# Kernel optimization log

Measured on AMD Instinct MI355X. Metric: run time of the kernel, lower is better.

The kernel has to match this reference:

```python
import jax, jax.numpy as jnp
import numpy as np

D_IN, D_HID, D_CLS, N_CLASSES = 1024, 256, 128, 4
CELL_IN = 512
N = 50000


def setup_inputs() -> dict:
    key = jax.random.key(0)
    ks = jax.random.split(key, 20)
    s = 0.02
    inp = {
        "x_path": jax.random.normal(ks[0], (1, N, D_IN), jnp.float32),
        "x_cell": jax.random.normal(ks[1], (1, N, CELL_IN), jnp.float32),
        # wsi_net / cell_net projections
        "wsi_w": jax.random.normal(ks[2], (D_IN, D_HID), jnp.float32) * s,
        "wsi_b": jnp.zeros((D_HID,), jnp.float32),
        "cell_w": jax.random.normal(ks[3], (CELL_IN, D_HID), jnp.float32) * s,
        "cell_b": jnp.zeros((D_HID,), jnp.float32),
        # cross-attention Q/K/V
        "wq_w": jax.random.normal(ks[4], (D_HID, D_HID), jnp.float32) * s,
        "wq_b": jnp.zeros((D_HID,), jnp.float32),
        "wk_w": jax.random.normal(ks[5], (D_HID, D_HID), jnp.float32) * s,
        "wk_b": jnp.zeros((D_HID,), jnp.float32),
        "wv_w": jax.random.normal(ks[6], (D_HID, D_HID), jnp.float32) * s,
        "wv_b": jnp.zeros((D_HID,), jnp.float32),
        # gated attention (L=D=256, n_classes=1)
        "aa_w": jax.random.normal(ks[7], (D_HID, D_HID), jnp.float32) * s,
        "aa_b": jnp.zeros((D_HID,), jnp.float32),
        "ab_w": jax.random.normal(ks[8], (D_HID, D_HID), jnp.float32) * s,
        "ab_b": jnp.zeros((D_HID,), jnp.float32),
        "ac_w": jax.random.normal(ks[9], (D_HID, 1), jnp.float32) * s,
        "ac_b": jnp.zeros((1,), jnp.float32),
        # classifier MLP
        "c1_w": jax.random.normal(ks[10], (D_HID, D_CLS), jnp.float32) * s,
        "c1_b": jnp.zeros((D_CLS,), jnp.float32),
        "c2_w": jax.random.normal(ks[11], (D_CLS, N_CLASSES), jnp.float32) * s,
        "c2_b": jnp.zeros((N_CLASSES,), jnp.float32),
    }
    return inp


def reference(x_path, x_cell, wsi_w, wsi_b, cell_w, cell_b,
              wq_w, wq_b, wk_w, wk_b, wv_w, wv_b,
              aa_w, aa_b, ab_w, ab_b, ac_w, ac_b,
              c1_w, c1_b, c2_w, c2_b):
    xp = x_path[0]            # (N, D_IN)
    xc = x_cell[0]            # (N, CELL_IN)
    # instance-level projections (dropout inactive at eval)
    h_path = jax.nn.relu(xp @ wsi_w + wsi_b)    # (N, d)
    h_cell = jax.nn.relu(xc @ cell_w + cell_b)  # (N, d)
    # cross attention with per-instance seq_len=1 (bmm over N singleton batches)
    q = h_cell @ wq_w + wq_b
    k = h_path @ wk_w + wk_b
    v = h_path @ wv_w + wv_b
    scores = (jnp.einsum('nd,nd->n', q, k) / jnp.sqrt(jnp.float32(q.shape[-1])))[:, None, None]  # (N,1,1)
    attn_w = jax.nn.softmax(scores, axis=-1)     # (N,1,1), trivially ones
    fused = attn_w[:, 0, :] * v                  # (N, d)
    # gated attention MIL pooling
    a = jnp.tanh(fused @ aa_w + aa_b)
    b = jax.nn.sigmoid(fused @ ab_w + ab_b)
    A = (a * b) @ ac_w + ac_b                    # (N, 1)
    A_t = A.T                                    # (1, N)
    pooled = jax.nn.softmax(A_t, axis=1) @ fused # (1, d)
    # classifier MLP
    risk = jax.nn.relu(pooled @ c1_w + c1_b) @ c2_w + c2_b  # (1, n_classes)
    return risk
```

## Files before the change

kernel.cpp:

```cpp
#include <hip/hip_runtime.h>
#include <hip/hip_bf16.h>
#include <math.h>

#define D_IN 1024
#define D_HID 256
#define D_CLS 128
#define N_CLASSES 4
#define N_INST 50000

#define ROWS 64
#define NBLK ((N_INST + ROWS - 1) / ROWS)
#define NB2 64
#define CHUNK ((NBLK + NB2 - 1) / NB2)
#define NEG_BIG (-1e30f)

typedef __attribute__((ext_vector_type(8))) short bf16x8;
typedef __attribute__((ext_vector_type(4))) float f32x4;

__global__ void convert_weights(const float* __restrict__ w1, const float* __restrict__ wv,
                                const float* __restrict__ wa, const float* __restrict__ wb,
                                __hip_bfloat16* __restrict__ w1t, __hip_bfloat16* __restrict__ wvt,
                                __hip_bfloat16* __restrict__ wat, __hip_bfloat16* __restrict__ wbt) {
    int idx = blockIdx.x * 256 + threadIdx.x;
    if (idx < D_IN * D_HID) {
        int k = idx >> 8;
        int n = idx & 255;
        w1t[(size_t)n * D_IN + k] = __float2bfloat16(w1[idx]);
    }
    if (idx < D_HID * D_HID) {
        int k = idx >> 8, n = idx & 255;
        wvt[n * D_HID + k] = __float2bfloat16(wv[idx]);
        wat[n * D_HID + k] = __float2bfloat16(wa[idx]);
        wbt[n * D_HID + k] = __float2bfloat16(wb[idx]);
    }
}

__device__ __forceinline__ void gemm256(const __hip_bfloat16 (*S)[264],
                                        const __hip_bfloat16* __restrict__ Wt,
                                        int wave, int quad, int l16, f32x4 acc[4][4]) {
    f32x4 zero = {0.f, 0.f, 0.f, 0.f};
#pragma unroll
    for (int i = 0; i < 4; i++)
#pragma unroll
        for (int j = 0; j < 4; j++) acc[i][j] = zero;
#pragma unroll
    for (int ks = 0; ks < 8; ks++) {
        bf16x8 af[4];
#pragma unroll
        for (int rt = 0; rt < 4; rt++)
            af[rt] = *(const bf16x8*)&S[rt * 16 + l16][ks * 32 + quad * 8];
#pragma unroll
        for (int ct = 0; ct < 4; ct++) {
            bf16x8 bf = *(const bf16x8*)(Wt + (size_t)(wave * 64 + ct * 16 + l16) * D_HID + ks * 32 + quad * 8);
#pragma unroll
            for (int rt = 0; rt < 4; rt++)
                acc[rt][ct] = __builtin_amdgcn_mfma_f32_16x16x32_bf16(af[rt], bf, acc[rt][ct], 0, 0, 0);
        }
    }
}

__launch_bounds__(256, 2)
__global__ void mcat_main(const float* __restrict__ xp,
                          const __hip_bfloat16* __restrict__ w1t, const float* __restrict__ b1,
                          const __hip_bfloat16* __restrict__ wvt, const float* __restrict__ bv,
                          const __hip_bfloat16* __restrict__ wat, const float* __restrict__ ba,
                          const __hip_bfloat16* __restrict__ wbt, const float* __restrict__ bb,
                          const float* __restrict__ acw, const float* __restrict__ acb,
                          float* __restrict__ partials) {
    __shared__ __hip_bfloat16 Xs[ROWS][72];
    __shared__ __hip_bfloat16 Hs[ROWS][264];
    __shared__ __hip_bfloat16 Vs[ROWS][264];
    __shared__ float Apart[4][ROWS];
    __shared__ float ExpW[ROWS];

    const int tid  = threadIdx.x;
    const int wave = tid >> 6;
    const int lane = tid & 63;
    const int quad = lane >> 4;
    const int l16  = lane & 15;
    const int row0 = blockIdx.x * ROWS;

    f32x4 acc[4][4];
    f32x4 zero = {0.f, 0.f, 0.f, 0.f};
#pragma unroll
    for (int i = 0; i < 4; i++)
#pragma unroll
        for (int j = 0; j < 4; j++) acc[i][j] = zero;

    for (int kc = 0; kc < D_IN; kc += 64) {
#pragma unroll
        for (int i = 0; i < 4; i++) {
            int lin = (i << 8) + tid;
            int r = lin >> 4;
            int c4 = (lin & 15) << 2;
            int grow = row0 + r;
            float4 xv = {0.f, 0.f, 0.f, 0.f};
            if (grow < N_INST) xv = *(const float4*)(xp + (size_t)grow * D_IN + kc + c4);
            Xs[r][c4 + 0] = __float2bfloat16(xv.x);
            Xs[r][c4 + 1] = __float2bfloat16(xv.y);
            Xs[r][c4 + 2] = __float2bfloat16(xv.z);
            Xs[r][c4 + 3] = __float2bfloat16(xv.w);
        }
        __syncthreads();
#pragma unroll
        for (int ks = 0; ks < 2; ks++) {
            bf16x8 af[4];
#pragma unroll
            for (int rt = 0; rt < 4; rt++)
                af[rt] = *(const bf16x8*)&Xs[rt * 16 + l16][ks * 32 + quad * 8];
#pragma unroll
            for (int ct = 0; ct < 4; ct++) {
                bf16x8 bf = *(const bf16x8*)(w1t + (size_t)(wave * 64 + ct * 16 + l16) * D_IN + kc + ks * 32 + quad * 8);
#pragma unroll
                for (int rt = 0; rt < 4; rt++)
                    acc[rt][ct] = __builtin_amdgcn_mfma_f32_16x16x32_bf16(af[rt], bf, acc[rt][ct], 0, 0, 0);
            }
        }
        __syncthreads();
    }
#pragma unroll
    for (int ct = 0; ct < 4; ct++) {
        int col = wave * 64 + ct * 16 + l16;
        float bias = b1[col];
#pragma unroll
        for (int rt = 0; rt < 4; rt++)
#pragma unroll
            for (int r = 0; r < 4; r++) {
                int row = rt * 16 + quad * 4 + r;
                float h = acc[rt][ct][r] + bias;
                Hs[row][col] = __float2bfloat16(fmaxf(h, 0.f));
            }
    }
    __syncthreads();

    gemm256(Hs, wvt, wave, quad, l16, acc);
#pragma unroll
    for (int ct = 0; ct < 4; ct++) {
        int col = wave * 64 + ct * 16 + l16;
        float bias = bv[col];
#pragma unroll
        for (int rt = 0; rt < 4; rt++)
#pragma unroll
            for (int r = 0; r < 4; r++) {
                int row = rt * 16 + quad * 4 + r;
                Vs[row][col] = __float2bfloat16(acc[rt][ct][r] + bias);
            }
    }
    __syncthreads();

    gemm256(Vs, wat, wave, quad, l16, acc);
#pragma unroll
    for (int ct = 0; ct < 4; ct++) {
        int col = wave * 64 + ct * 16 + l16;
        float bias = ba[col];
#pragma unroll
        for (int rt = 0; rt < 4; rt++)
#pragma unroll
            for (int r = 0; r < 4; r++) {
                int row = rt * 16 + quad * 4 + r;
                Hs[row][col] = __float2bfloat16(tanhf(acc[rt][ct][r] + bias));
            }
    }

    gemm256(Vs, wbt, wave, quad, l16, acc);
#pragma unroll
    for (int ct = 0; ct < 4; ct++) {
        int col = wave * 64 + ct * 16 + l16;
        float bias = bb[col];
#pragma unroll
        for (int rt = 0; rt < 4; rt++)
#pragma unroll
            for (int r = 0; r < 4; r++) {
                int row = rt * 16 + quad * 4 + r;
                float bval = 1.f / (1.f + __expf(-(acc[rt][ct][r] + bias)));
                float aval = __bfloat162float(Hs[row][col]);
                Hs[row][col] = __float2bfloat16(aval * bval);
            }
    }
    __syncthreads();

    {
        int r = tid & 63;
        int dg = tid >> 6;
        float s = 0.f;
#pragma unroll 8
        for (int d = 0; d < 64; d++) {
            int col = dg * 64 + d;
            s += __bfloat162float(Hs[r][col]) * acw[col];
        }
        Apart[dg][r] = s;
    }
    __syncthreads();

    if (tid < 64) {
        bool valid = (row0 + tid) < N_INST;
        float A = Apart[0][tid] + Apart[1][tid] + Apart[2][tid] + Apart[3][tid] + acb[0];
        if (!valid) A = NEG_BIG;
        float m = A;
#pragma unroll
        for (int off = 32; off > 0; off >>= 1) m = fmaxf(m, __shfl_xor(m, off));
        float e = valid ? __expf(A - m) : 0.f;
        ExpW[tid] = e;
        float ssum = e;
#pragma unroll
        for (int off = 32; off > 0; off >>= 1) ssum += __shfl_xor(ssum, off);
        if (tid == 0) {
            partials[(size_t)blockIdx.x * 258 + 0] = m;
            partials[(size_t)blockIdx.x * 258 + 1] = ssum;
        }
    }
    __syncthreads();
    {
        float p = 0.f;
#pragma unroll 8
        for (int n = 0; n < 64; n++)
            p += ExpW[n] * __bfloat162float(Vs[n][tid]);
        partials[(size_t)blockIdx.x * 258 + 2 + tid] = p;
    }
}

__global__ void mcat_fin_a(const float* __restrict__ p1, float* __restrict__ p2) {
    __shared__ float sm[1];
    int g = blockIdx.x, tid = threadIdx.x;
    int lo = g * CHUNK;
    int hi = lo + CHUNK; if (hi > NBLK) hi = NBLK;
    if (tid < 64) {
        float m = NEG_BIG;
        if (lo + tid < hi) m = p1[(size_t)(lo + tid) * 258];
#pragma unroll
        for (int off = 32; off > 0; off >>= 1) m = fmaxf(m, __shfl_xor(m, off));
        if (tid == 0) sm[0] = m;
    }
    __syncthreads();
    float M = sm[0];
    float p = 0.f, sacc = 0.f;
    for (int b = lo; b < hi; b++) {
        float sc = __expf(p1[(size_t)b * 258] - M);
        sacc += sc * p1[(size_t)b * 258 + 1];
        p += sc * p1[(size_t)b * 258 + 2 + tid];
    }
    if (tid == 0) {
        p2[(size_t)g * 258 + 0] = M;
        p2[(size_t)g * 258 + 1] = sacc;
    }
    p2[(size_t)g * 258 + 2 + tid] = p;
}

__global__ void mcat_fin_b(const float* __restrict__ p2,
                           const float* __restrict__ c1w, const float* __restrict__ c1b,
                           const float* __restrict__ c2w, const float* __restrict__ c2b,
                           float* __restrict__ out) {
    __shared__ float sm[2];
    __shared__ float sc[NB2];
    __shared__ float pooled[D_HID];
    __shared__ float r1[D_CLS];
    int tid = threadIdx.x;
    if (tid < 64) {
        float m = p2[(size_t)tid * 258];
#pragma unroll
        for (int off = 32; off > 0; off >>= 1) m = fmaxf(m, __shfl_xor(m, off));
        if (tid == 0) sm[0] = m;
    }
    __syncthreads();
    float M = sm[0];
    if (tid < 64) {
        float s = __expf(p2[(size_t)tid * 258] - M);
        sc[tid] = s;
        float Ssum = s * p2[(size_t)tid * 258 + 1];
#pragma unroll
        for (int off = 32; off > 0; off >>= 1) Ssum += __shfl_xor(Ssum, off);
        if (tid == 0) sm[1] = Ssum;
    }
    __syncthreads();
    float S = sm[1];
    float p = 0.f;
#pragma unroll 8
    for (int b = 0; b < NB2; b++)
        p += sc[b] * p2[(size_t)b * 258 + 2 + tid];
    pooled[tid] = p / S;
    __syncthreads();
    if (tid < D_CLS) {
        float acc = c1b[tid];
#pragma unroll 8
        for (int d = 0; d < D_HID; d++)
            acc += pooled[d] * c1w[(size_t)d * D_CLS + tid];
        r1[tid] = fmaxf(acc, 0.f);
    }
    __syncthreads();
    if (tid < N_CLASSES) {
        float acc = c2b[tid];
#pragma unroll 8
        for (int j = 0; j < D_CLS; j++)
            acc += r1[j] * c2w[(size_t)j * N_CLASSES + tid];
        out[tid] = acc;
    }
}

extern "C" void kernel_launch(void* const* d_in, const int* in_sizes, int n_in,
                              void* d_out, int out_size, void* d_ws, size_t ws_size,
                              hipStream_t stream) {
    const float* xp  = (const float*)d_in[0];
    const float* w1  = (const float*)d_in[2];
    const float* b1  = (const float*)d_in[3];
    const float* wv  = (const float*)d_in[10];
    const float* bv  = (const float*)d_in[11];
    const float* wa  = (const float*)d_in[12];
    const float* ba  = (const float*)d_in[13];
    const float* wb  = (const float*)d_in[14];
    const float* bb  = (const float*)d_in[15];
    const float* acw = (const float*)d_in[16];
    const float* acb = (const float*)d_in[17];
    const float* c1w = (const float*)d_in[18];
    const float* c1b = (const float*)d_in[19];
    const float* c2w = (const float*)d_in[20];
    const float* c2b = (const float*)d_in[21];
    float* out = (float*)d_out;

    char* ws = (char*)d_ws;
    __hip_bfloat16* w1t = (__hip_bfloat16*)(ws);
    __hip_bfloat16* wvt = (__hip_bfloat16*)(ws + 524288);
    __hip_bfloat16* wat = (__hip_bfloat16*)(ws + 655360);
    __hip_bfloat16* wbt = (__hip_bfloat16*)(ws + 786432);
    float* p1 = (float*)(ws + 917504);
    float* p2 = (float*)(ws + 917504 + 807024);

    hipLaunchKernelGGL(convert_weights, dim3(1024), dim3(256), 0, stream,
                       w1, wv, wa, wb, w1t, wvt, wat, wbt);
    hipLaunchKernelGGL(mcat_main, dim3(NBLK), dim3(256), 0, stream,
                       xp, w1t, b1, wvt, bv, wat, ba, wbt, bb, acw, acb, p1);
    hipLaunchKernelGGL(mcat_fin_a, dim3(NB2), dim3(256), 0, stream, p1, p2);
    hipLaunchKernelGGL(mcat_fin_b, dim3(1), dim3(256), 0, stream,
                       p2, c1w, c1b, c2w, c2b, out);
}
```

Baseline: 540.2 us.

## Load x_path directly into MFMA fragments, tile weight transpose, use fast tanh/sigmoid

The first-layer GEMM stops staging x_path through shared memory. Each lane now loads eight fp32 values straight from global memory, converts them to bf16 and feeds them to MFMA, which removes the LDS round trip and the two __syncthreads per K-chunk. The weight conversion kernel now transposes through a shared-memory tile so its global writes are coalesced, and tanh and sigmoid use exp plus a reciprocal approximation. In exchange, each x row is fetched with a strided 32-byte access pattern per lane, which may reduce coalescing compared with the earlier float4 layout, and the fast activations lose a little precision.

```diff
diff --git a/kernel.cpp b/kernel.cpp
--- a/kernel.cpp
+++ b/kernel.cpp
@@ -17,21 +17,66 @@
 typedef __attribute__((ext_vector_type(8))) short bf16x8;
 typedef __attribute__((ext_vector_type(4))) float f32x4;
 
+__device__ __forceinline__ short f2bf(float x) {
+    __hip_bfloat16 h = __float2bfloat16(x);
+    return *reinterpret_cast<short*>(&h);
+}
+
+__device__ __forceinline__ float fast_tanh(float x) {
+    float e = __expf(2.f * x);
+    return 1.f - 2.f * __builtin_amdgcn_rcpf(e + 1.f);
+}
+__device__ __forceinline__ float fast_sigmoid(float x) {
+    return __builtin_amdgcn_rcpf(1.f + __expf(-x));
+}
+
+__device__ __forceinline__ bf16x8 load_cvt8(const float* __restrict__ p) {
+    float4 a = *(const float4*)p;
+    float4 b = *(const float4*)(p + 4);
+    bf16x8 r;
+    r[0] = f2bf(a.x); r[1] = f2bf(a.y); r[2] = f2bf(a.z); r[3] = f2bf(a.w);
+    r[4] = f2bf(b.x); r[5] = f2bf(b.y); r[6] = f2bf(b.z); r[7] = f2bf(b.w);
+    return r;
+}
+
 __global__ void convert_weights(const float* __restrict__ w1, const float* __restrict__ wv,
                                 const float* __restrict__ wa, const float* __restrict__ wb,
                                 __hip_bfloat16* __restrict__ w1t, __hip_bfloat16* __restrict__ wvt,
                                 __hip_bfloat16* __restrict__ wat, __hip_bfloat16* __restrict__ wbt) {
-    int idx = blockIdx.x * 256 + threadIdx.x;
-    if (idx < D_IN * D_HID) {
-        int k = idx >> 8;
-        int n = idx & 255;
-        w1t[(size_t)n * D_IN + k] = __float2bfloat16(w1[idx]);
-    }
-    if (idx < D_HID * D_HID) {
-        int k = idx >> 8, n = idx & 255;
-        wvt[n * D_HID + k] = __float2bfloat16(wv[idx]);
-        wat[n * D_HID + k] = __float2bfloat16(wa[idx]);
-        wbt[n * D_HID + k] = __float2bfloat16(wb[idx]);
+    __shared__ __hip_bfloat16 T[64][68];
+    int b = blockIdx.x, tid = threadIdx.x;
+    const float* src; __hip_bfloat16* dst; int K, tr, tc;
+    if (b < 64) { src = w1; dst = w1t; K = D_IN; tr = b >> 2; tc = b & 3; }
+    else {
+        int m = (b - 64) >> 4, t = (b - 64) & 15;
+        src = (m == 0) ? wv : (m == 1) ? wa : wb;
+        dst = (m == 0) ? wvt : (m == 1) ? wat : wbt;
+        K = D_HID; tr = t >> 2; tc = t & 3;
+    }
+    int k0 = tr * 64, n0 = tc * 64;
+#pragma unroll
+    for (int p = 0; p < 4; p++) {
+        int lin = p * 256 + tid;
+        int r = lin >> 4;
+        int c4 = (lin & 15) << 2;
+        float4 v = *(const float4*)(src + (size_t)(k0 + r) * D_HID + n0 + c4);
+        T[c4 + 0][r] = __float2bfloat16(v.x);
+        T[c4 + 1][r] = __float2bfloat16(v.y);
+        T[c4 + 2][r] = __float2bfloat16(v.z);
+        T[c4 + 3][r] = __float2bfloat16(v.w);
+    }
+    __syncthreads();
+#pragma unroll
+    for (int p = 0; p < 4; p++) {
+        int lin = p * 256 + tid;
+        int n = lin >> 4;
+        int kq = (lin & 15) << 2;
+        ushort4 o;
+        o.x = *(unsigned short*)&T[n][kq + 0];
+        o.y = *(unsigned short*)&T[n][kq + 1];
+        o.z = *(unsigned short*)&T[n][kq + 2];
+        o.w = *(unsigned short*)&T[n][kq + 3];
+        *(ushort4*)(dst + (size_t)(n0 + n) * K + k0 + kq) = o;
     }
 }
 
@@ -51,10 +96,10 @@
             af[rt] = *(const bf16x8*)&S[rt * 16 + l16][ks * 32 + quad * 8];
 #pragma unroll
         for (int ct = 0; ct < 4; ct++) {
-            bf16x8 bf = *(const bf16x8*)(Wt + (size_t)(wave * 64 + ct * 16 + l16) * D_HID + ks * 32 + quad * 8);
+            bf16x8 bfv = *(const bf16x8*)(Wt + (size_t)(wave * 64 + ct * 16 + l16) * D_HID + ks * 32 + quad * 8);
 #pragma unroll
             for (int rt = 0; rt < 4; rt++)
-                acc[rt][ct] = __builtin_amdgcn_mfma_f32_16x16x32_bf16(af[rt], bf, acc[rt][ct], 0, 0, 0);
+                acc[rt][ct] = __builtin_amdgcn_mfma_f32_16x16x32_bf16(af[rt], bfv, acc[rt][ct], 0, 0, 0);
         }
     }
 }
@@ -67,7 +112,6 @@
                           const __hip_bfloat16* __restrict__ wbt, const float* __restrict__ bb,
                           const float* __restrict__ acw, const float* __restrict__ acb,
                           float* __restrict__ partials) {
-    __shared__ __hip_bfloat16 Xs[ROWS][72];
     __shared__ __hip_bfloat16 Hs[ROWS][264];
     __shared__ __hip_bfloat16 Vs[ROWS][264];
     __shared__ float Apart[4][ROWS];
@@ -87,37 +131,37 @@
 #pragma unroll
         for (int j = 0; j < 4; j++) acc[i][j] = zero;
 
-    for (int kc = 0; kc < D_IN; kc += 64) {
-#pragma unroll
-        for (int i = 0; i < 4; i++) {
-            int lin = (i << 8) + tid;
-            int r = lin >> 4;
-            int c4 = (lin & 15) << 2;
-            int grow = row0 + r;
-            float4 xv = {0.f, 0.f, 0.f, 0.f};
-            if (grow < N_INST) xv = *(const float4*)(xp + (size_t)grow * D_IN + kc + c4);
-            Xs[r][c4 + 0] = __float2bfloat16(xv.x);
-            Xs[r][c4 + 1] = __float2bfloat16(xv.y);
-            Xs[r][c4 + 2] = __float2bfloat16(xv.z);
-            Xs[r][c4 + 3] = __float2bfloat16(xv.w);
+    const float* xbase[4];
+#pragma unroll
+    for (int rt = 0; rt < 4; rt++) {
+        int r = row0 + rt * 16 + l16;
+        if (r > N_INST - 1) r = N_INST - 1;
+        xbase[rt] = xp + (size_t)r * D_IN + quad * 8;
+    }
+    const __hip_bfloat16* wbase[4];
+#pragma unroll
+    for (int ct = 0; ct < 4; ct++)
+        wbase[ct] = w1t + (size_t)(wave * 64 + ct * 16 + l16) * D_IN + quad * 8;
+
+    for (int ko = 0; ko < 8; ko++) {
+#pragma unroll
+        for (int ki = 0; ki < 4; ki++) {
+            const int kc = (ko * 4 + ki) * 32;
+            bf16x8 af[4];
+#pragma unroll
+            for (int rt = 0; rt < 4; rt++)
+                af[rt] = load_cvt8(xbase[rt] + kc);
+#pragma unroll
+            for (int ct = 0; ct < 4; ct++) {
+                bf16x8 bfv = *(const bf16x8*)(wbase[ct] + kc);
+#pragma unroll
+                for (int rt = 0; rt < 4; rt++)
+                    acc[rt][ct] = __builtin_amdgcn_mfma_f32_16x16x32_bf16(af[rt], bfv, acc[rt][ct], 0, 0, 0);
+            }
         }
-        __syncthreads();
-#pragma unroll
-        for (int ks = 0; ks < 2; ks++) {
-            bf16x8 af[4];
-#pragma unroll
-            for (int rt = 0; rt < 4; rt++)
-                af[rt] = *(const bf16x8*)&Xs[rt * 16 + l16][ks * 32 + quad * 8];
-#pragma unroll
-            for (int ct = 0; ct < 4; ct++) {
-                bf16x8 bf = *(const bf16x8*)(w1t + (size_t)(wave * 64 + ct * 16 + l16) * D_IN + kc + ks * 32 + quad * 8);
-#pragma unroll
-                for (int rt = 0; rt < 4; rt++)
-                    acc[rt][ct] = __builtin_amdgcn_mfma_f32_16x16x32_bf16(af[rt], bf, acc[rt][ct], 0, 0, 0);
-            }
-        }
-        __syncthreads();
-    }
+        __builtin_amdgcn_s_barrier();
+    }
+
 #pragma unroll
     for (int ct = 0; ct < 4; ct++) {
         int col = wave * 64 + ct * 16 + l16;
@@ -158,7 +202,7 @@
 #pragma unroll
             for (int r = 0; r < 4; r++) {
                 int row = rt * 16 + quad * 4 + r;
-                Hs[row][col] = __float2bfloat16(tanhf(acc[rt][ct][r] + bias));
+                Hs[row][col] = __float2bfloat16(fast_tanh(acc[rt][ct][r] + bias));
             }
     }
 
@@ -172,7 +216,7 @@
 #pragma unroll
             for (int r = 0; r < 4; r++) {
                 int row = rt * 16 + quad * 4 + r;
-                float bval = 1.f / (1.f + __expf(-(acc[rt][ct][r] + bias)));
+                float bval = fast_sigmoid(acc[rt][ct][r] + bias);
                 float aval = __bfloat162float(Hs[row][col]);
                 Hs[row][col] = __float2bfloat16(aval * bval);
             }
@@ -324,7 +368,7 @@
     float* p1 = (float*)(ws + 917504);
     float* p2 = (float*)(ws + 917504 + 807024);
 
-    hipLaunchKernelGGL(convert_weights, dim3(1024), dim3(256), 0, stream,
+    hipLaunchKernelGGL(convert_weights, dim3(112), dim3(256), 0, stream,
                        w1, wv, wa, wb, w1t, wvt, wat, wbt);
     hipLaunchKernelGGL(mcat_main, dim3(NBLK), dim3(256), 0, stream,
                        xp, w1t, b1, wvt, bv, wat, ba, wbt, bb, acw, acb, p1);
```

Result: no change. 545.7 us (+1.0%).
